# Kernel optimization log

Hardware: AMD Instinct MI355X
Metric: run time of the kernel (lower is better)

The kernel has to match this reference:

```python
import jax, jax.numpy as jnp
import numpy as np

HEADS = 16
HEAD_DIM = 128
ROPE_BASE = 10000.0

def _rope_tables(T, D):
    # inv_freq over even indices, freqs = outer(pos, inv_freq), emb = concat([freqs, freqs])
    inv_freq = 1.0 / (ROPE_BASE ** (jnp.arange(0, D, 2, dtype=jnp.float32) / D))
    t = jnp.arange(T, dtype=jnp.float32)
    freqs = t[:, None] * inv_freq[None, :]          # (T, D/2)
    emb = jnp.concatenate([freqs, freqs], axis=-1)  # (T, D)
    return jnp.cos(emb), jnp.sin(emb)

def _rotate_half(x):
    half = x.shape[-1] // 2
    x1, x2 = x[..., :half], x[..., half:]
    return jnp.concatenate([-x2, x1], axis=-1)

def setup_inputs() -> dict:
    key = jax.random.key(0)
    k1, k2, k3 = jax.random.split(key, 3)
    B, T, dim = 2, 2048, 2048
    inner = HEADS * HEAD_DIM
    x = jax.random.normal(k1, (B, T, dim), dtype=jnp.float32)
    W_qkv = jax.random.normal(k2, (3 * inner, dim), dtype=jnp.float32) * 0.02
    W_proj = jax.random.normal(k3, (dim, inner), dtype=jnp.float32) * 0.02
    return {"x": x, "W_qkv": W_qkv, "W_proj": W_proj}

def reference(x, W_qkv, W_proj):
    B, T, dim = x.shape
    H, D = HEADS, HEAD_DIM
    # QKV projection (Linear with weight (out, in): y = x @ W^T)
    qkv = jnp.einsum('btd,ed->bte', x, W_qkv)          # (B, T, 3*H*D)
    q, k, v = jnp.split(qkv, 3, axis=-1)
    def to_heads(t):
        return t.reshape(B, T, H, D).transpose(0, 2, 1, 3)  # (B, H, T, D)
    q, k, v = to_heads(q), to_heads(k), to_heads(v)
    # RoPE, offset = 0 (uncached path)
    cos, sin = _rope_tables(T, D)                      # (T, D)
    cos = cos[None, None]
    sin = sin[None, None]
    q = q * cos + _rotate_half(q) * sin
    k = k * cos + _rotate_half(k) * sin
    # causal SDPA
    scale = 1.0 / jnp.sqrt(jnp.float32(D))
    scores = jnp.einsum('bhqd,bhkd->bhqk', q, k) * scale
    causal = jnp.tril(jnp.ones((T, T), dtype=bool))
    scores = jnp.where(causal[None, None], scores, jnp.finfo(scores.dtype).min)
    attn = jax.nn.softmax(scores, axis=-1)
    out = jnp.einsum('bhqk,bhkd->bhqd', attn, v)       # (B, H, T, D)
    out = out.transpose(0, 2, 1, 3).reshape(B, T, H * D)
    return jnp.einsum('bti,oi->bto', out, W_proj)      # (B, T, dim)
```

## Files before the change

### kernel.cpp

```cpp
#include <hip/hip_runtime.h>
#include <hip/hip_bf16.h>
#include <stdint.h>

typedef __attribute__((ext_vector_type(8))) short short8;
typedef __attribute__((ext_vector_type(4))) short short4v;
typedef __attribute__((ext_vector_type(4))) float f32x4;

#define HEADS 16
#define HDIM  128
#define BB    2
#define TT    2048
#define DMODEL 2048
#define INNER 2048
#define E3    6144
#define NTOK  (BB*TT)

__device__ inline void store1(__hip_bfloat16* p, float v) { *p = __float2bfloat16(v); }
__device__ inline void store1(float* p, float v)          { *p = v; }

__device__ inline short bfbits(float v) {
  __hip_bfloat16 h = __float2bfloat16(v);
  return *(short*)&h;
}

__device__ inline void gl_lds16(const __hip_bfloat16* g, __hip_bfloat16* l) {
  __builtin_amdgcn_global_load_lds(
      (const __attribute__((address_space(1))) void*)g,
      (__attribute__((address_space(3))) void*)l, 16, 0, 0);
}

__device__ inline void cvt8(const float* in, __hip_bfloat16* out, int i) {
  float4 a = *(const float4*)(in + i);
  float4 b = *(const float4*)(in + i + 4);
  short8 r;
  r[0]=bfbits(a.x); r[1]=bfbits(a.y); r[2]=bfbits(a.z); r[3]=bfbits(a.w);
  r[4]=bfbits(b.x); r[5]=bfbits(b.y); r[6]=bfbits(b.z); r[7]=bfbits(b.w);
  *(short8*)(out + i) = r;
}

#define NBX   (NTOK*DMODEL/2048)
#define NBW   (E3*DMODEL/2048)
#define NBT   (TT*64/256)
__global__ __launch_bounds__(256)
void prep(const float* __restrict__ x, const float* __restrict__ Wqkv,
          __hip_bfloat16* __restrict__ xb, __hip_bfloat16* __restrict__ Wqkvb,
          float2* __restrict__ tab)
{
  const int tid = threadIdx.x;
  int blk = blockIdx.x;
  if (blk < NBX) {
    cvt8(x, xb, (blk*256 + tid)*8);
  } else if (blk < NBX + NBW) {
    cvt8(Wqkv, Wqkvb, ((blk-NBX)*256 + tid)*8);
  } else {
    int idx = (blk - NBX - NBW)*256 + tid;
    int t  = idx >> 6;
    int d2 = idx & 63;
    float inv = powf(10000.f, -(float)d2 * (1.f/64.f));
    float ang = (float)t * inv;
    tab[idx] = make_float2(cosf(ang), sinf(ang));
  }
}

__global__ __launch_bounds__(256)
void cvt_bf16(const float* __restrict__ in, __hip_bfloat16* __restrict__ out, int n)
{
  int i = (blockIdx.x * 256 + threadIdx.x) * 8;
  if (i >= n) return;
  cvt8(in, out, i);
}

template<typename TC>
__global__ __launch_bounds__(256, 2)
void gemm_lds(const __hip_bfloat16* __restrict__ A,
              const __hip_bfloat16* __restrict__ B,
              TC* __restrict__ C,
              int M, int N, int K)
{
  __shared__ __hip_bfloat16 sA[128*32];
  __shared__ __hip_bfloat16 sB[128*32];
  const int tid  = threadIdx.x;
  const int lane = tid & 63;
  const int wv   = tid >> 6;
  const int lm   = lane & 15;
  const int quad = lane >> 4;
  const int wm   = (wv >> 1) * 64;
  const int wn   = (wv & 1) * 64;
  const int bm   = blockIdx.y * 128;
  const int bn   = blockIdx.x * 128;

  f32x4 acc[4][4];
  #pragma unroll
  for (int i=0;i<4;i++)
    #pragma unroll
    for (int j=0;j<4;j++) acc[i][j] = (f32x4){0.f,0.f,0.f,0.f};

  const int srow = wv*32 + (lane >> 2);
  const int scol = (lane & 3) * 8;
  const __hip_bfloat16* gA0 = A + (size_t)(bm + srow)*K + scol;
  const __hip_bfloat16* gA1 = gA0 + (size_t)16*K;
  const __hip_bfloat16* gB0 = B + (size_t)(bn + srow)*K + scol;
  const __hip_bfloat16* gB1 = gB0 + (size_t)16*K;
  __hip_bfloat16* lA0 = sA + wv*1024;
  __hip_bfloat16* lA1 = lA0 + 512;
  __hip_bfloat16* lB0 = sB + wv*1024;
  __hip_bfloat16* lB1 = lB0 + 512;

  for (int k0 = 0; k0 < K; k0 += 32) {
    __syncthreads();
    gl_lds16(gA0, lA0);
    gl_lds16(gA1, lA1);
    gl_lds16(gB0, lB0);
    gl_lds16(gB1, lB1);
    gA0 += 32; gA1 += 32; gB0 += 32; gB1 += 32;
    __syncthreads();
    short8 af[4], bf[4];
    #pragma unroll
    for (int t=0;t<4;t++)
      af[t] = *(const short8*)(sA + (wm + t*16 + lm)*32 + quad*8);
    #pragma unroll
    for (int t=0;t<4;t++)
      bf[t] = *(const short8*)(sB + (wn + t*16 + lm)*32 + quad*8);
    #pragma unroll
    for (int i=0;i<4;i++)
      #pragma unroll
      for (int j=0;j<4;j++)
        acc[i][j] = __builtin_amdgcn_mfma_f32_16x16x32_bf16(af[i], bf[j], acc[i][j], 0,0,0);
  }

  const int row0 = bm + wm + quad*4;
  const int col0 = bn + wn + lm;
  #pragma unroll
  for (int i=0;i<4;i++)
    #pragma unroll
    for (int j=0;j<4;j++)
      #pragma unroll
      for (int r=0;r<4;r++)
        store1(C + (size_t)(row0 + i*16 + r)*N + col0 + j*16, acc[i][j][r]);
}

__global__ __launch_bounds__(512, 2)
void gemm_qkv3(const __hip_bfloat16* __restrict__ A,
               const __hip_bfloat16* __restrict__ B,
               const float2* __restrict__ tab,
               __hip_bfloat16* __restrict__ Qh,
               __hip_bfloat16* __restrict__ Kh,
               __hip_bfloat16* __restrict__ Vt)
{
  __shared__ __align__(128) __hip_bfloat16 smem[49152];
  const int tid  = threadIdx.x;
  const int lane = tid & 63;
  const int w    = tid >> 6;
  const int lm   = lane & 15;
  const int quad = lane >> 4;
  const int wm   = w >> 2;
  const int wn   = w & 3;

  const int flat  = blockIdx.x;
  const int wgid  = (flat & 7) * 96 + (flat >> 3);
  const int tileN = wgid >> 5;
  const int tileM = wgid & 31;
  const int bm    = tileM << 7;
  const int bn    = tileN << 8;
  const int type  = bn >> 11;

  const int r0 = tid >> 3;
  const int kc = (tid & 7) ^ (r0 & 7);
  const size_t gA0 = ((size_t)(bm      + r0) << 11) + kc*8;
  const size_t gA1 = ((size_t)(bm + 64 + r0) << 11) + kc*8;
  size_t gB[2][2];
  #pragma unroll
  for (int h = 0; h < 2; ++h)
    #pragma unroll
    for (int j = 0; j < 2; ++j) {
      int prow;
      if (type < 2)
        prow = h*128 + j*32 + ((r0 >> 5) << 6) + (((r0 >> 4) & 1) << 4) + (r0 & 15);
      else
        prow = h*128 + j*64 + r0;
      gB[h][j] = ((size_t)(bn + prow) << 11) + kc*8;
    }
  const int ldsW = w * 512;

#define STAGE_A(ktt, bb_) do { \
    __hip_bfloat16* _l = smem + (bb_)*24576 + ldsW; \
    gl_lds16(A + gA0 + (size_t)(ktt)*64, _l); \
    gl_lds16(A + gA1 + (size_t)(ktt)*64, _l + 4096); \
  } while (0)
#define STAGE_B(h, ktt, bb_) do { \
    __hip_bfloat16* _l = smem + (bb_)*24576 + 8192 + (h)*8192 + ldsW; \
    gl_lds16(B + gB[h][0] + (size_t)(ktt)*64, _l); \
    gl_lds16(B + gB[h][1] + (size_t)(ktt)*64, _l + 4096); \
  } while (0)

  const int xk0 = ((quad      ^ (lm & 7)) << 3);
  const int xk1 = (((quad|4)  ^ (lm & 7)) << 3);
  const int aRow = wm*4096 + lm*64;
  const int bRow = 8192 + (wn>>1)*8192 + (wn&1)*4096 + lm*64;

  f32x4 acc[4][4];
  #pragma unroll
  for (int i=0;i<4;i++)
    #pragma unroll
    for (int j=0;j<4;j++) acc[i][j] = (f32x4){0.f,0.f,0.f,0.f};

  STAGE_A(0, 0);
  STAGE_B(0, 0, 0);
  STAGE_B(1, 0, 0);
  STAGE_A(1, 1);
  asm volatile("s_waitcnt vmcnt(2)" ::: "memory");
  __builtin_amdgcn_s_barrier();

  #pragma unroll 2
  for (int kt = 0; kt < 32; ++kt) {
    const int cb   = kt & 1;
    const int nb   = cb ^ 1;
    const int cOff = cb * 24576;

    short8 a0[4], b0[4], a1[4], b1[4];
    #pragma unroll
    for (int f = 0; f < 4; ++f) {
      a0[f] = *(const short8*)(smem + cOff + aRow + f*1024 + xk0);
      b0[f] = *(const short8*)(smem + cOff + bRow + f*1024 + xk0);
    }
    #pragma unroll
    for (int f = 0; f < 4; ++f) {
      a1[f] = *(const short8*)(smem + cOff + aRow + f*1024 + xk1);
      b1[f] = *(const short8*)(smem + cOff + bRow + f*1024 + xk1);
    }
    if (kt + 1 < 32) STAGE_B(0, kt+1, nb);
    __builtin_amdgcn_s_barrier();
    __builtin_amdgcn_s_setprio(1);
    #pragma unroll
    for (int i = 0; i < 4; ++i)
      #pragma unroll
      for (int j = 0; j < 4; ++j)
        acc[i][j] = __builtin_amdgcn_mfma_f32_16x16x32_bf16(a0[i], b0[j], acc[i][j], 0,0,0);
    __builtin_amdgcn_s_setprio(0);
    __builtin_amdgcn_s_barrier();

    if (kt + 1 < 32) STAGE_B(1, kt+1, nb);
    if (kt + 2 < 32) STAGE_A(kt+2, cb);
    __builtin_amdgcn_s_barrier();
    __builtin_amdgcn_s_setprio(1);
    #pragma unroll
    for (int i = 0; i < 4; ++i)
      #pragma unroll
      for (int j = 0; j < 4; ++j)
        acc[i][j] = __builtin_amdgcn_mfma_f32_16x16x32_bf16(a1[i], b1[j], acc[i][j], 0,0,0);
    __builtin_amdgcn_s_setprio(0);
    if (kt < 30) asm volatile("s_waitcnt vmcnt(2)" ::: "memory");
    else         asm volatile("s_waitcnt vmcnt(0)" ::: "memory");
    __builtin_amdgcn_s_barrier();
  }
#undef STAGE_A
#undef STAGE_B

  const float SCQ = 0.08838834764831845f * 1.4426950408889634f;
  const int tok0 = bm + wm*64;
  if (type < 2) {
    __hip_bfloat16* const dst = (type == 0) ? Qh : Kh;
    const float mul = (type == 0) ? SCQ : 1.0f;
    const int head = ((bn & 2047) >> 7) + (wn >> 1);
    const int d2b  = (wn & 1)*32 + lm;
    #pragma unroll
    for (int i = 0; i < 4; ++i) {
      #pragma unroll
      for (int r = 0; r < 4; ++r) {
        const int t  = tok0 + i*16 + quad*4 + r;
        const int b  = t >> 11;
        const int tl = t & (TT-1);
        const float2* tp = tab + (size_t)tl*64;
        __hip_bfloat16* const o = dst + ((size_t)(b*HEADS + head)*TT + tl)*HDIM;
        #pragma unroll
        for (int j = 0; j < 2; ++j) {
          const int d2 = d2b + j*16;
          const float2 cs = tp[d2];
          const float v1 = acc[i][j  ][r];
          const float v2 = acc[i][j+2][r];
          o[d2]      = __float2bfloat16((v1*cs.x - v2*cs.y) * mul);
          o[d2 + 64] = __float2bfloat16((v2*cs.x + v1*cs.y) * mul);
        }
      }
    }
  } else {
    const int fcb = (bn & 2047) + wn*64 + lm;
    #pragma unroll
    for (int i = 0; i < 4; ++i) {
      const int t0 = tok0 + i*16 + quad*4;
      const int b  = t0 >> 11;
      const int tl = t0 & (TT-1);
      #pragma unroll
      for (int j = 0; j < 4; ++j) {
        const int c    = fcb + j*16;
        const int head = c >> 7;
        const int d    = c & 127;
        short4v o;
        #pragma unroll
        for (int r = 0; r < 4; ++r) o[r] = bfbits(acc[i][j][r]);
        *(short4v*)(Vt + ((size_t)(b*HEADS + head)*HDIM + d)*TT + tl) = o;
      }
    }
  }
}

__global__ __launch_bounds__(256, 3)
void flash_attn(const __hip_bfloat16* __restrict__ Qh,
                const __hip_bfloat16* __restrict__ Kh,
                const __hip_bfloat16* __restrict__ Vt,
                __hip_bfloat16* __restrict__ Out)
{
  const int tid  = threadIdx.x;
  const int lane = tid & 63;
  const int wv   = tid >> 6;
  const int lm   = lane & 15;
  const int quad = lane >> 4;
  const int jA   = blockIdx.x;
  const int bh   = blockIdx.y;
  const int b    = bh >> 4;
  const int h    = bh & 15;

  __shared__ __hip_bfloat16 sK[64*136];
  __shared__ __hip_bfloat16 sV[128*72];
  __shared__ __hip_bfloat16 sP[4][16*72];

  const float FML2 = 8.0f * 1.4426950408889634f;

  const int rk0 = tid >> 4;
  const int ck  = (tid & 15) * 8;
  const int dv0 = tid >> 3;
  const int cv  = (tid & 7) * 8;
  const __hip_bfloat16* KpBase = Kh + (size_t)bh*TT*HDIM + (size_t)rk0*HDIM + ck;
  const __hip_bfloat16* VpBase = Vt + (size_t)bh*HDIM*TT + (size_t)dv0*TT + cv;

  #pragma unroll
  for (int pass = 0; pass < 2; ++pass) {
    const int q0 = (pass == 0 ? jA : 31 - jA) * 64;

    short8 aq[4];
    {
      const __hip_bfloat16* qp = Qh + ((size_t)bh*TT + q0 + wv*16 + lm)*HDIM + quad*8;
      #pragma unroll
      for (int kd=0;kd<4;kd++) aq[kd] = *(const short8*)(qp + kd*32);
    }

    float l_p[4] = {0,0,0,0};
    f32x4 acc_o[8];
    #pragma unroll
    for (int i=0;i<8;i++) acc_o[i] = (f32x4){0.f,0.f,0.f,0.f};

    const __hip_bfloat16* Kp = KpBase;
    const __hip_bfloat16* Vp = VpBase;
    short8 pk[4], pv[4];
    #pragma unroll
    for (int it=0;it<4;++it) {
      pk[it] = *(const short8*)(Kp + (size_t)it*16*HDIM);
      pv[it] = *(const short8*)(Vp + (size_t)it*32*TT);
    }
    Kp += (size_t)64*HDIM; Vp += 64;

    for (int kv0 = 0; kv0 <= q0; kv0 += 64) {
      __syncthreads();
      #pragma unroll
      for (int it=0;it<4;++it) {
        *(short8*)(&sK[(it*16 + rk0)*136 + ck]) = pk[it];
        *(short8*)(&sV[(it*32 + dv0)*72 + cv])  = pv[it];
      }
      if (kv0 + 64 <= q0) {
        #pragma unroll
        for (int it=0;it<4;++it) {
          pk[it] = *(const short8*)(Kp + (size_t)it*16*HDIM);
          pv[it] = *(const short8*)(Vp + (size_t)it*32*TT);
        }
        Kp += (size_t)64*HDIM; Vp += 64;
      }
      __syncthreads();

      f32x4 accs[4];
      #pragma unroll
      for (int nt=0;nt<4;nt++) accs[nt] = (f32x4){0.f,0.f,0.f,0.f};
      #pragma unroll
      for (int kd=0;kd<4;kd++)
        #pragma unroll
        for (int nt=0;nt<4;nt++) {
          short8 bk = *(const short8*)(&sK[(nt*16 + lm)*136 + kd*32 + quad*8]);
          accs[nt] = __builtin_amdgcn_mfma_f32_16x16x32_bf16(aq[kd], bk, accs[nt], 0,0,0);
        }

      const int rowb = q0 + wv*16 + quad*4;
      const bool diag = (kv0 == q0);
      #pragma unroll
      for (int nt=0;nt<4;nt++)
        #pragma unroll
        for (int r=0;r<4;r++) {
          float p = exp2f(accs[nt][r] - FML2);
          if (diag && (kv0 + nt*16 + lm > rowb + r)) p = 0.f;
          l_p[r] += p;
          sP[wv][(quad*4 + r)*72 + nt*16 + lm] = __float2bfloat16(p);
        }

      #pragma unroll
      for (int kd2=0;kd2<2;kd2++) {
        short8 ap = *(const short8*)(&sP[wv][lm*72 + kd2*32 + quad*8]);
        #pragma unroll
        for (int nt2=0;nt2<8;nt2++) {
          short8 bvv = *(const short8*)(&sV[(nt2*16 + lm)*72 + kd2*32 + quad*8]);
          acc_o[nt2] = __builtin_amdgcn_mfma_f32_16x16x32_bf16(ap, bvv, acc_o[nt2], 0,0,0);
        }
      }
    }

    #pragma unroll
    for (int off=1; off<16; off<<=1)
      #pragma unroll
      for (int r=0;r<4;r++) l_p[r] += __shfl_xor(l_p[r], off);
    #pragma unroll
    for (int r=0;r<4;r++) l_p[r] = 1.f / l_p[r];

    #pragma unroll
    for (int nt2=0;nt2<8;nt2++)
      #pragma unroll
      for (int r=0;r<4;r++) {
        int t = q0 + wv*16 + quad*4 + r;
        Out[((size_t)b*TT + t)*INNER + (size_t)h*HDIM + nt2*16 + lm] =
          __float2bfloat16(acc_o[nt2][r] * l_p[r]);
      }
  }
}

extern "C" void kernel_launch(void* const* d_in, const int* in_sizes, int n_in,
                              void* d_out, int out_size, void* d_ws, size_t ws_size,
                              hipStream_t stream)
{
  (void)in_sizes; (void)n_in; (void)out_size; (void)ws_size;
  const float* x     = (const float*)d_in[0];
  const float* Wqkv  = (const float*)d_in[1];
  const float* Wproj = (const float*)d_in[2];
  float* out = (float*)d_out;

  char* ws = (char*)d_ws;
  __hip_bfloat16* xb       = (__hip_bfloat16*)ws;
  __hip_bfloat16* attn_out = xb;
  char* p1 = ws + (size_t)NTOK*DMODEL*2;
  __hip_bfloat16* Wqkvb  = (__hip_bfloat16*)p1;
  __hip_bfloat16* Wprojb = (__hip_bfloat16*)p1;
  char* p2 = p1 + (size_t)E3*DMODEL*2;
  float2* ropeTab = (float2*)p2;
  char* p3 = p2 + (size_t)DMODEL*INNER*2;
  const size_t hsz = (size_t)BB*HEADS*TT*HDIM*2;
  __hip_bfloat16* Qh = (__hip_bfloat16*)p3;
  __hip_bfloat16* Kh = (__hip_bfloat16*)(p3 + hsz);
  __hip_bfloat16* Vt = (__hip_bfloat16*)(p3 + 2*hsz);

  prep<<<dim3(NBX + NBW + NBT), dim3(256), 0, stream>>>(x, Wqkv, xb, Wqkvb, ropeTab);

  gemm_qkv3<<<dim3(768), dim3(512), 0, stream>>>(xb, Wqkvb, ropeTab, Qh, Kh, Vt);

  cvt_bf16<<<dim3(DMODEL*INNER/2048), dim3(256), 0, stream>>>(Wproj, Wprojb, DMODEL*INNER);

  flash_attn<<<dim3(TT/128, BB*HEADS), dim3(256), 0, stream>>>(Qh, Kh, Vt, attn_out);

  gemm_lds<float>
    <<<dim3(INNER/128, NTOK/128), dim3(256), 0, stream>>>(attn_out, Wprojb, out, NTOK, INNER, DMODEL);
}
```

Before: 378.4 us.

## Load K/V directly from global in attention, drop LDS staging and barriers

The attention kernel no longer stages K and V tiles through shared memory with double-buffered register prefetch and two barriers per iteration. Each wave now reads its K and V MFMA operands straight from global memory, which is meant to rely on L2/L1 cache hits. The grid is flattened and remapped so that consecutive workgroups spread across 8 groups (XCD-style swizzle), and s_setprio is raised around the MFMA sequences. Redundant global reads by the four waves and exposed load latency are the main risks.

```diff
diff --git a/kernel.cpp b/kernel.cpp
--- a/kernel.cpp
+++ b/kernel.cpp
@@ -305,33 +305,29 @@
 }
 
 __global__ __launch_bounds__(256, 3)
-void flash_attn(const __hip_bfloat16* __restrict__ Qh,
-                const __hip_bfloat16* __restrict__ Kh,
-                const __hip_bfloat16* __restrict__ Vt,
-                __hip_bfloat16* __restrict__ Out)
+void flash_attn2(const __hip_bfloat16* __restrict__ Qh,
+                 const __hip_bfloat16* __restrict__ Kh,
+                 const __hip_bfloat16* __restrict__ Vt,
+                 __hip_bfloat16* __restrict__ Out)
 {
   const int tid  = threadIdx.x;
   const int lane = tid & 63;
   const int wv   = tid >> 6;
   const int lm   = lane & 15;
   const int quad = lane >> 4;
-  const int jA   = blockIdx.x;
-  const int bh   = blockIdx.y;
+  const int flat = blockIdx.x;
+  const int wgid = (flat & 7) * 64 + (flat >> 3);
+  const int jA   = wgid & 15;
+  const int bh   = wgid >> 4;
   const int b    = bh >> 4;
   const int h    = bh & 15;
 
-  __shared__ __hip_bfloat16 sK[64*136];
-  __shared__ __hip_bfloat16 sV[128*72];
   __shared__ __hip_bfloat16 sP[4][16*72];
 
   const float FML2 = 8.0f * 1.4426950408889634f;
 
-  const int rk0 = tid >> 4;
-  const int ck  = (tid & 15) * 8;
-  const int dv0 = tid >> 3;
-  const int cv  = (tid & 7) * 8;
-  const __hip_bfloat16* KpBase = Kh + (size_t)bh*TT*HDIM + (size_t)rk0*HDIM + ck;
-  const __hip_bfloat16* VpBase = Vt + (size_t)bh*HDIM*TT + (size_t)dv0*TT + cv;
+  const __hip_bfloat16* const Kb = Kh + (size_t)bh*TT*HDIM;
+  const __hip_bfloat16* const Vb = Vt + (size_t)bh*HDIM*TT;
 
   #pragma unroll
   for (int pass = 0; pass < 2; ++pass) {
@@ -349,43 +345,24 @@
     #pragma unroll
     for (int i=0;i<8;i++) acc_o[i] = (f32x4){0.f,0.f,0.f,0.f};
 
-    const __hip_bfloat16* Kp = KpBase;
-    const __hip_bfloat16* Vp = VpBase;
-    short8 pk[4], pv[4];
-    #pragma unroll
-    for (int it=0;it<4;++it) {
-      pk[it] = *(const short8*)(Kp + (size_t)it*16*HDIM);
-      pv[it] = *(const short8*)(Vp + (size_t)it*32*TT);
-    }
-    Kp += (size_t)64*HDIM; Vp += 64;
-
     for (int kv0 = 0; kv0 <= q0; kv0 += 64) {
-      __syncthreads();
-      #pragma unroll
-      for (int it=0;it<4;++it) {
-        *(short8*)(&sK[(it*16 + rk0)*136 + ck]) = pk[it];
-        *(short8*)(&sV[(it*32 + dv0)*72 + cv])  = pv[it];
-      }
-      if (kv0 + 64 <= q0) {
-        #pragma unroll
-        for (int it=0;it<4;++it) {
-          pk[it] = *(const short8*)(Kp + (size_t)it*16*HDIM);
-          pv[it] = *(const short8*)(Vp + (size_t)it*32*TT);
-        }
-        Kp += (size_t)64*HDIM; Vp += 64;
-      }
-      __syncthreads();
-
       f32x4 accs[4];
       #pragma unroll
       for (int nt=0;nt<4;nt++) accs[nt] = (f32x4){0.f,0.f,0.f,0.f};
+      __builtin_amdgcn_s_setprio(1);
       #pragma unroll
       for (int kd=0;kd<4;kd++)
         #pragma unroll
         for (int nt=0;nt<4;nt++) {
-          short8 bk = *(const short8*)(&sK[(nt*16 + lm)*136 + kd*32 + quad*8]);
+          short8 bk = *(const short8*)(Kb + (size_t)(kv0 + nt*16 + lm)*HDIM + kd*32 + quad*8);
           accs[nt] = __builtin_amdgcn_mfma_f32_16x16x32_bf16(aq[kd], bk, accs[nt], 0,0,0);
         }
+      __builtin_amdgcn_s_setprio(0);
+
+      short8 bv0[8];
+      #pragma unroll
+      for (int nt2=0;nt2<8;nt2++)
+        bv0[nt2] = *(const short8*)(Vb + (size_t)(nt2*16 + lm)*TT + kv0 + quad*8);
 
       const int rowb = q0 + wv*16 + quad*4;
       const bool diag = (kv0 == q0);
@@ -399,15 +376,20 @@
           sP[wv][(quad*4 + r)*72 + nt*16 + lm] = __float2bfloat16(p);
         }
 
-      #pragma unroll
-      for (int kd2=0;kd2<2;kd2++) {
-        short8 ap = *(const short8*)(&sP[wv][lm*72 + kd2*32 + quad*8]);
-        #pragma unroll
-        for (int nt2=0;nt2<8;nt2++) {
-          short8 bvv = *(const short8*)(&sV[(nt2*16 + lm)*72 + kd2*32 + quad*8]);
-          acc_o[nt2] = __builtin_amdgcn_mfma_f32_16x16x32_bf16(ap, bvv, acc_o[nt2], 0,0,0);
-        }
+      short8 ap0 = *(const short8*)(&sP[wv][lm*72 + quad*8]);
+      __builtin_amdgcn_s_setprio(1);
+      #pragma unroll
+      for (int nt2=0;nt2<8;nt2++)
+        acc_o[nt2] = __builtin_amdgcn_mfma_f32_16x16x32_bf16(ap0, bv0[nt2], acc_o[nt2], 0,0,0);
+      __builtin_amdgcn_s_setprio(0);
+      short8 ap1 = *(const short8*)(&sP[wv][lm*72 + 32 + quad*8]);
+      __builtin_amdgcn_s_setprio(1);
+      #pragma unroll
+      for (int nt2=0;nt2<8;nt2++) {
+        short8 bv = *(const short8*)(Vb + (size_t)(nt2*16 + lm)*TT + kv0 + 32 + quad*8);
+        acc_o[nt2] = __builtin_amdgcn_mfma_f32_16x16x32_bf16(ap1, bv, acc_o[nt2], 0,0,0);
       }
+      __builtin_amdgcn_s_setprio(0);
     }
 
     #pragma unroll
@@ -458,7 +440,7 @@
 
   cvt_bf16<<<dim3(DMODEL*INNER/2048), dim3(256), 0, stream>>>(Wproj, Wprojb, DMODEL*INNER);
 
-  flash_attn<<<dim3(TT/128, BB*HEADS), dim3(256), 0, stream>>>(Qh, Kh, Vt, attn_out);
+  flash_attn2<<<dim3(512), dim3(256), 0, stream>>>(Qh, Kh, Vt, attn_out);
 
   gemm_lds<float>
     <<<dim3(INNER/128, NTOK/128), dim3(256), 0, stream>>>(attn_out, Wprojb, out, NTOK, INNER, DMODEL);
```

Result: slower. 527.3 us (+39.4%).
